# Performance work log

Measured on AMD Instinct MI355X. Metric: run time of the kernel, lower is better.

## Reference

```python
import jax, jax.numpy as jnp
import numpy as np

# dims (see shape_source): seq S = d_t+1 must equal d_k for the unary quantum loader
B, T, D_IN = 128, 127, 48
DK = 128
S = T + 1            # tokens incl. class token; S == DK
H, L = 8, 6
P = (S * S - S) // 2  # RBS angles per head (pyramid circuit over S wires)


def _pyramid_pairs(n):
    # deterministic pyramid ordering of n(n-1)/2 adjacent-pair Givens rotations
    a, b = [], []
    for k in range(n - 1):
        for i in range(k, -1, -1):
            a.append(i)
            b.append(i + 1)
    return np.asarray(a, np.int32), np.asarray(b, np.int32)


def _build_W(phi, pa, pb, n):
    # classical simulation of the RBS pyramid circuit restricted to the unary
    # subspace: product of Givens rotations -> orthogonal n x n matrix
    def step(W, inp):
        ia, ib, th = inp
        c, s = jnp.cos(th), jnp.sin(th)
        ra, rb = W[ia], W[ib]
        W = W.at[ia].set(c * ra - s * rb)
        W = W.at[ib].set(s * ra + c * rb)
        return W, None
    W0 = jnp.eye(n, dtype=phi.dtype)
    W, _ = jax.lax.scan(step, W0, (pa, pb, phi))
    return W


def _layer_norm(x, g, b, eps=1e-5):
    m = jnp.mean(x, axis=-1, keepdims=True)
    v = jnp.mean((x - m) ** 2, axis=-1, keepdims=True)
    return (x - m) * jax.lax.rsqrt(v + eps) * g + b


def setup_inputs() -> dict:
    key = jax.random.key(0)
    ks = jax.random.split(key, 8)
    f32 = jnp.float32
    return {
        "x": jax.random.normal(ks[0], (B, T, D_IN), f32),
        "embed_w": jax.random.normal(ks[1], (DK, D_IN), f32) / np.sqrt(D_IN),
        "embed_b": jnp.zeros((DK,), f32),
        "class_token": jax.random.normal(ks[2], (DK,), f32) / DK,
        "norm0_g": jnp.ones((DK,), f32),
        "norm0_b": jnp.zeros((DK,), f32),
        "Vw": jax.random.normal(ks[3], (L, H, DK, DK), f32) / np.sqrt(DK),
        "Vb": jnp.zeros((L, H, DK), f32),
        "ln_g": jnp.ones((L, H, DK), f32),
        "ln_b": jnp.zeros((L, H, DK), f32),
        "phi": jax.random.normal(ks[4], (L, H, P), f32) / np.sqrt(S),
        "merger_w": jax.random.normal(ks[5], (L, H), f32) / np.sqrt(H),
        "merger_b": jnp.zeros((L,), f32),
    }


def reference(x, embed_w, embed_b, class_token, norm0_g, norm0_b,
              Vw, Vb, ln_g, ln_b, phi, merger_w, merger_b):
    Bsz = x.shape[0]
    pa, pb = _pyramid_pairs(S)
    # orthogonal score matrices for every (layer, head)
    Ws = jax.vmap(lambda p: _build_W(p, pa, pb, S))(phi.reshape(L * H, P))
    Ws = Ws.reshape(L, H, S, S)

    # embed patches, prepend class token (pos_embedding add is a no-op in the
    # original source: bare `+self.pos_embedding` statement, so it is omitted)
    tok = jnp.einsum('btf,df->btd', x, embed_w) + embed_b
    h = jnp.concatenate([jnp.broadcast_to(class_token, (Bsz, 1, DK)), tok], axis=1)
    h = _layer_norm(h, norm0_g, norm0_b)

    scale = 1.0 / np.sqrt(DK)
    for l in range(L):
        nrm = jnp.sqrt(jnp.sum(h * h, axis=-1))      # input3: token norms [B,S]
        u = h / nrm[..., None]                        # unit tokens (convert_array)
        hh, nn, uu = h, nrm, u

        def head(W, vw, vb, g, be):
            V = jnp.einsum('bsd,ed->bse', hh, vw) + vb
            M = jnp.einsum('bsd,de,bte->bst', uu, W, uu)
            A = (M * M) * (nn[:, :, None] * nn[:, None, :])
            Pm = jax.nn.softmax(A * scale, axis=-1)
            return _layer_norm(jnp.einsum('bst,btd->bsd', Pm, V) + hh, g, be)

        hs = jax.vmap(head)(Ws[l], Vw[l], Vb[l], ln_g[l], ln_b[l])  # [H,B,S,D]
        h = jnp.einsum('hbsd,h->bsd', hs, merger_w[l]) + merger_b[l]
    return h[:, -1, :]
```

## Files before the change

kernel.cpp:

```cpp
#include <hip/hip_runtime.h>
#include <hip/hip_bf16.h>


typedef __bf16 bf16x8 __attribute__((ext_vector_type(8)));
typedef float  f32x4  __attribute__((ext_vector_type(4)));
typedef unsigned int u32;

__device__ __forceinline__ int sidx(int row, int col)
{
    return row * 128 + ((((col >> 3) ^ (row & 15)) << 3) | (col & 7));
}

__global__ void __launch_bounds__(256)
prep_kernel(const float* __restrict__ phi, float2* __restrict__ csn,
            const float* __restrict__ vw,  __bf16* __restrict__ cvwf)
{
    if (blockIdx.x < 3072) {
        const int mat = blockIdx.x >> 6;
        const int t   = ((blockIdx.x & 63) << 2) + (threadIdx.x >> 6);
        const int j   = threadIdx.x & 63;
        float th = 0.f;
        if (t < 253) {
            const int p = t & 1, i = 2 * j + p;
            const int lim = min(t, 252 - t);
            if (i <= lim) {
                const int k = (t + i) >> 1;
                th = phi[mat * 8128 + ((k * (k + 1)) >> 1) + (k - i)];
            }
        }
        float sn, cs;
        __sincosf(th, &sn, &cs);
        csn[(mat * 256 + t) * 64 + j] = make_float2(cs, sn);
    } else {
        const int f    = (blockIdx.x - 3072) * 256 + threadIdx.x;
        const int lane = f & 63;
        const int k0   = (f >> 6) & 3;
        const int t    = (f >> 8) & 7;
        const int lh   = f >> 11;
        const int row  = t * 16 + (lane & 15);
        const int col  = k0 * 32 + (lane >> 4) * 8;
        const float* src = vw + (lh * 128 + row) * 128 + col;
        __bf16* dst = cvwf + f * 8;
#pragma unroll
        for (int j = 0; j < 8; j++) dst[j] = (__bf16)src[j];
    }
}

__global__ void __launch_bounds__(64)
build_w_kernel(const float2* __restrict__ csn, __bf16* __restrict__ wtf)
{
    const int mat = blockIdx.x >> 5;
    const int grp = blockIdx.x & 31;
    const int c0  = grp * 4;
    const int lam = threadIdx.x;

    const float2* base = csn + (mat * 256) * 64 + lam;

    float vlo[4], vhi[4];
#pragma unroll
    for (int j = 0; j < 4; j++) {
        vlo[j] = (2 * lam     == c0 + j) ? 1.f : 0.f;
        vhi[j] = (2 * lam + 1 == c0 + j) ? 1.f : 0.f;
    }

    float2 buf[3][16];
#pragma unroll
    for (int k = 0; k < 16; k++) buf[0][k] = base[k * 64];
#pragma unroll
    for (int k = 0; k < 16; k++) buf[1][k] = base[(16 + k) * 64];

#pragma unroll
    for (int g = 0; g < 16; g++) {
        const int cb = g % 3;
        if (g < 14) {
            const int nb = (g + 2) % 3;
#pragma unroll
            for (int k = 0; k < 16; k++)
                buf[nb][k] = base[((g + 2) * 16 + k) * 64];
        }
#pragma unroll
        for (int p = 0; p < 8; p++) {
            {
                const float cs = buf[cb][2 * p].x, sn = buf[cb][2 * p].y;
#pragma unroll
                for (int j = 0; j < 4; j++) {
                    float lo = vlo[j], hi = vhi[j];
                    vlo[j] = cs * lo - sn * hi;
                    vhi[j] = sn * lo + cs * hi;
                }
            }
            {
                const float cs = buf[cb][2 * p + 1].x, sn = buf[cb][2 * p + 1].y;
#pragma unroll
                for (int j = 0; j < 4; j++) {
                    float y  = __shfl_down(vlo[j], 1);
                    float x  = vhi[j];
                    float xn = cs * x - sn * y;
                    float yn = sn * x + cs * y;
                    vhi[j] = xn;
                    float z = __shfl_up(yn, 1);
                    if (lam > 0) vlo[j] = z;
                }
            }
        }
    }

    u32* wtu = (u32*)wtf;
#pragma unroll
    for (int j = 0; j < 4; j++) {
        const int c = c0 + j;
        __bf16 va = (__bf16)vlo[j];
        __bf16 vb = (__bf16)vhi[j];
        u32 pk = (u32)__builtin_bit_cast(unsigned short, va)
               | ((u32)__builtin_bit_cast(unsigned short, vb) << 16);
        const int idx = (((c >> 4) * 4 + (lam >> 4)) * 64
                         + ((lam >> 2) & 3) * 16 + (c & 15)) * 4 + (lam & 3);
        wtu[mat * 8192 + idx] = pk;
    }
}

__global__ void __launch_bounds__(512)
embed_kernel(const float* __restrict__ x,  const float* __restrict__ ew,
             const float* __restrict__ eb, const float* __restrict__ ct,
             const float* __restrict__ g0, const float* __restrict__ b0,
             float* __restrict__ hf, __bf16* __restrict__ hb,
             float* __restrict__ invn)
{
    __shared__ float sx[4][48];
    __shared__ float sred[4][2];
    const int d  = threadIdx.x & 127, sq = threadIdx.x >> 7;
    const int wh = (threadIdx.x >> 6) & 1;
    const int b  = blockIdx.x & 127;
    const int s  = (blockIdx.x >> 7) * 4 + sq;

    if (s > 0 && d < 48) sx[sq][d] = x[(b * 127 + (s - 1)) * 48 + d];
    __syncthreads();

    float val;
    if (s == 0) {
        val = ct[d];
    } else {
        float aa = 0.f;
#pragma unroll
        for (int f = 0; f < 48; f++) aa = fmaf(sx[sq][f], ew[d * 48 + f], aa);
        val = aa + eb[d];
    }
    float v = val;
#pragma unroll
    for (int m = 32; m; m >>= 1) v += __shfl_xor(v, m);
    if ((threadIdx.x & 63) == 0) sred[sq][wh] = v;
    __syncthreads();
    float mean = (sred[sq][0] + sred[sq][1]) * (1.f / 128.f);
    float xc   = val - mean;
    __syncthreads();
    v = xc * xc;
#pragma unroll
    for (int m = 32; m; m >>= 1) v += __shfl_xor(v, m);
    if ((threadIdx.x & 63) == 0) sred[sq][wh] = v;
    __syncthreads();
    float var = (sred[sq][0] + sred[sq][1]) * (1.f / 128.f);
    float y   = xc * rsqrtf(var + 1e-5f) * g0[d] + b0[d];
    __syncthreads();
    v = y * y;
#pragma unroll
    for (int m = 32; m; m >>= 1) v += __shfl_xor(v, m);
    if ((threadIdx.x & 63) == 0) sred[sq][wh] = v;
    __syncthreads();
    float ss = sred[sq][0] + sred[sq][1];

    const int o = (b * 128 + s) * 128 + d;
    hf[o] = y;
    hb[o] = (__bf16)y;
    if (d == 0) invn[b * 128 + s] = rsqrtf(ss);
}

__global__ void __launch_bounds__(512, 4)
attn_kernel(int l,
            const float*  __restrict__ hf,  const __bf16* __restrict__ hb,
            const float*  __restrict__ invn, const __bf16* __restrict__ wtf,
            const __bf16* __restrict__ vwf, const float* __restrict__ vb,
            const float* __restrict__ lng,  const float* __restrict__ lnb,
            const float* __restrict__ mwp,  __bf16* __restrict__ hs)
{
    __shared__ __align__(16) __bf16 sH[128 * 128];
    __shared__ __align__(16) __bf16 sY[128 * 128];
    __shared__ float sInv[128];
    __shared__ float sVb[128];
    __shared__ float sLg[128];
    __shared__ float sLb[128];

    const int tid  = threadIdx.x;
    const int lane = tid & 63, w = tid >> 6;
    const int l15  = lane & 15, quad = lane >> 4;
    const int b    = blockIdx.x & 127;
    const int hh   = blockIdx.x >> 7;
    const int lh   = l * 8 + hh;

    const __bf16* hbp = hb + b * 16384;

#pragma unroll
    for (int c = 0; c < 4; c++) {
        int ch  = tid + c * 512;
        int row = ch >> 4, cc = ch & 15;
        bf16x8 hv = *(const bf16x8*)(hbp + ch * 8);
        *(bf16x8*)(&sH[sidx(row, cc * 8)]) = hv;
    }
    if (tid < 128) {
        sInv[tid] = invn[b * 128 + tid];
        sVb[tid]  = vb[lh * 128 + tid];
        sLg[tid]  = lng[lh * 128 + tid];
        sLb[tid]  = lnb[lh * 128 + tid];
    }
    __syncthreads();

    const int r0 = w * 16;
    const int kq = quad * 8;
    const int q4 = quad * 4;
    const f32x4 vzero = {0.f, 0.f, 0.f, 0.f};

    f32x4 acc[8];

    auto mmG = [&](const __bf16* gbase) {
#pragma unroll
        for (int t = 0; t < 8; t++) acc[t] = vzero;
        const __bf16* gp = gbase + lane * 8;
#pragma unroll
        for (int k0c = 0; k0c < 4; k0c++) {
            bf16x8 a0 = *(const bf16x8*)(&sH[sidx(r0 + l15, k0c * 32 + kq)]);
#pragma unroll
            for (int t = 0; t < 8; t++) {
                bf16x8 bb = *(const bf16x8*)(gp + (t * 4 + k0c) * 512);
                acc[t] = __builtin_amdgcn_mfma_f32_16x16x32_bf16(a0, bb, acc[t], 0, 0, 0);
            }
        }
    };
    auto mmL = [&]() {
#pragma unroll
        for (int t = 0; t < 8; t++) acc[t] = vzero;
#pragma unroll
        for (int k0 = 0; k0 < 128; k0 += 32) {
            const int kk = k0 + kq;
            bf16x8 a0 = *(const bf16x8*)(&sY[sidx(r0 + l15, kk)]);
#pragma unroll
            for (int t = 0; t < 8; t++) {
                bf16x8 bb = *(const bf16x8*)(&sH[sidx(t * 16 + l15, kk)]);
                acc[t] = __builtin_amdgcn_mfma_f32_16x16x32_bf16(a0, bb, acc[t], 0, 0, 0);
            }
        }
    };

    mmG(wtf + (size_t)lh * 16384);
#pragma unroll
    for (int t = 0; t < 8; t++)
#pragma unroll
        for (int r = 0; r < 4; r++)
            sY[sidx(r0 + q4 + r, t * 16 + l15)] = (__bf16)acc[t][r];

    mmL();

    {
        const float scale2 = 0.08838834764831843f * 1.4426950408889634f;
        float invt[8];
#pragma unroll
        for (int t = 0; t < 8; t++) invt[t] = sInv[t * 16 + l15];
        float invs[4];
#pragma unroll
        for (int r = 0; r < 4; r++) invs[r] = sInv[r0 + q4 + r];

        float mx[4] = {-3e38f, -3e38f, -3e38f, -3e38f};
#pragma unroll
        for (int t = 0; t < 8; t++)
#pragma unroll
            for (int r = 0; r < 4; r++) {
                float g = acc[t][r];
                float v = g * g * invs[r] * invt[t] * scale2;
                acc[t][r] = v;
                mx[r] = fmaxf(mx[r], v);
            }
#pragma unroll
        for (int m = 1; m < 16; m <<= 1)
#pragma unroll
            for (int r = 0; r < 4; r++) mx[r] = fmaxf(mx[r], __shfl_xor(mx[r], m));

        float sm[4] = {0.f, 0.f, 0.f, 0.f};
#pragma unroll
        for (int t = 0; t < 8; t++)
#pragma unroll
            for (int r = 0; r < 4; r++) {
                float e = exp2f(acc[t][r] - mx[r]);
                acc[t][r] = e;
                sm[r] += e;
            }
#pragma unroll
        for (int m = 1; m < 16; m <<= 1)
#pragma unroll
            for (int r = 0; r < 4; r++) sm[r] += __shfl_xor(sm[r], m);
#pragma unroll
        for (int r = 0; r < 4; r++) sm[r] = 1.0f / sm[r];
#pragma unroll
        for (int t = 0; t < 8; t++)
#pragma unroll
            for (int r = 0; r < 4; r++)
                sY[sidx(r0 + q4 + r, t * 16 + l15)] = (__bf16)(acc[t][r] * sm[r]);
    }

    float hres[8][4];
    {
        const float* hfp = hf + (b * 128 + r0 + q4) * 128;
#pragma unroll
        for (int t = 0; t < 8; t++)
#pragma unroll
            for (int r = 0; r < 4; r++)
                hres[t][r] = hfp[r * 128 + t * 16 + l15];
    }

    mmG(vwf + (size_t)lh * 16384);
    __syncthreads();

    {
        float vbv[8];
#pragma unroll
        for (int t = 0; t < 8; t++) vbv[t] = sVb[t * 16 + l15];
#pragma unroll
        for (int t = 0; t < 8; t++)
#pragma unroll
            for (int r = 0; r < 4; r++)
                sH[sidx(t * 16 + l15, r0 + q4 + r)] = (__bf16)(acc[t][r] + vbv[t]);
    }
    __syncthreads();

    mmL();

    {
        const float mw = mwp[lh];
        float lgv[8], lbv[8];
#pragma unroll
        for (int t = 0; t < 8; t++) {
            lgv[t] = sLg[t * 16 + l15];
            lbv[t] = sLb[t * 16 + l15];
        }
        float sum_[4] = {0.f, 0.f, 0.f, 0.f};
        float sq_[4]  = {0.f, 0.f, 0.f, 0.f};
#pragma unroll
        for (int t = 0; t < 8; t++)
#pragma unroll
            for (int r = 0; r < 4; r++) {
                float xx = acc[t][r] + hres[t][r];
                acc[t][r] = xx;
                sum_[r] += xx;
                sq_[r]  += xx * xx;
            }
#pragma unroll
        for (int m = 1; m < 16; m <<= 1)
#pragma unroll
            for (int r = 0; r < 4; r++) {
                sum_[r] += __shfl_xor(sum_[r], m);
                sq_[r]  += __shfl_xor(sq_[r], m);
            }
        float mean[4], rstd[4];
#pragma unroll
        for (int r = 0; r < 4; r++) {
            mean[r] = sum_[r] * (1.f / 128.f);
            float var = sq_[r] * (1.f / 128.f) - mean[r] * mean[r];
            rstd[r] = rsqrtf(fmaxf(var, 0.f) + 1e-5f);
        }
        __bf16* hsp = hs + ((hh * 128 + b) * 128 + r0 + q4) * 128;
#pragma unroll
        for (int t = 0; t < 8; t++)
#pragma unroll
            for (int r = 0; r < 4; r++) {
                float y = (acc[t][r] - mean[r]) * rstd[r] * lgv[t] + lbv[t];
                hsp[r * 128 + t * 16 + l15] = (__bf16)(y * mw);
            }
    }
}

static __device__ __forceinline__ float block_sum_128(float v, float* sred)
{
#pragma unroll
    for (int m = 32; m; m >>= 1) v += __shfl_xor(v, m);
    __syncthreads();
    if ((threadIdx.x & 63) == 0) sred[threadIdx.x >> 6] = v;
    __syncthreads();
    return sred[0] + sred[1];
}

__global__ void __launch_bounds__(128)
merge_kernel(const __bf16* __restrict__ hs, const float* __restrict__ mbp, int l,
             float* __restrict__ hf, __bf16* __restrict__ hb, float* __restrict__ invn,
             float* __restrict__ out, int last)
{
    __shared__ float sred[2];
    const int b = blockIdx.x & 127, s = blockIdx.x >> 7, d = threadIdx.x;

    float acc = mbp[l];
#pragma unroll
    for (int h = 0; h < 8; h++)
        acc += (float)hs[((h * 128 + b) * 128 + s) * 128 + d];

    float ss = block_sum_128(acc * acc, sred);

    const int o = (b * 128 + s) * 128 + d;
    hf[o] = acc;
    hb[o] = (__bf16)acc;
    if (d == 0) invn[b * 128 + s] = rsqrtf(ss);
    if (last && s == 127) out[b * 128 + d] = acc;
}

extern "C" void kernel_launch(void* const* d_in, const int* in_sizes, int n_in,
                              void* d_out, int out_size, void* d_ws, size_t ws_size,
                              hipStream_t stream)
{
    (void)in_sizes; (void)n_in; (void)out_size; (void)ws_size;

    const float* x   = (const float*)d_in[0];
    const float* ew  = (const float*)d_in[1];
    const float* eb  = (const float*)d_in[2];
    const float* ct  = (const float*)d_in[3];
    const float* g0  = (const float*)d_in[4];
    const float* b0  = (const float*)d_in[5];
    const float* vw  = (const float*)d_in[6];
    const float* vb  = (const float*)d_in[7];
    const float* lng = (const float*)d_in[8];
    const float* lnb = (const float*)d_in[9];
    const float* phi = (const float*)d_in[10];
    const float* mw  = (const float*)d_in[11];
    const float* mb  = (const float*)d_in[12];
    float* out = (float*)d_out;

    char* ws = (char*)d_ws;
    __bf16* wtf  = (__bf16*)(ws);
    float*  hf   = (float*)(ws + 1572864);
    __bf16* hb   = (__bf16*)(ws + 9961472);
    float*  invn = (float*)(ws + 14155776);
    __bf16* hs   = (__bf16*)(ws + 14221312);
    __bf16* cvwf = (__bf16*)(ws + 47775744);
    float2* csn  = (float2*)(ws + 49348608);

    prep_kernel<<<3456, 256, 0, stream>>>(phi, csn, vw, cvwf);
    build_w_kernel<<<1536, 64, 0, stream>>>(csn, wtf);
    embed_kernel<<<4096, 512, 0, stream>>>(x, ew, eb, ct, g0, b0, hf, hb, invn);
    for (int l = 0; l < 6; l++) {
        attn_kernel<<<1024, 512, 0, stream>>>(l, hf, hb, invn, wtf, cvwf, vb,
                                              lng, lnb, mw, hs);
        merge_kernel<<<16384, 128, 0, stream>>>(hs, mb, l, hf, hb, invn, out,
                                                (l == 5) ? 1 : 0);
    }
}
```

Measured before the change: 463.4 us.

## Stage rotation matrix in LDS for first GEMM and widen merge kernel work per block

The build kernel now writes W transposed in a plain row-major layout instead of MFMA fragment order. The attention kernel loads W into shared memory alongside H at kernel start and computes H·W from LDS rather than streaming fragments from global memory. This adds a barrier before overwriting sY. The merge kernel now handles four tokens per 256-thread block with two elements per thread, dropping the shared-memory block reduction in favour of a single wave shuffle and using vectorised stores.

```diff
diff --git a/kernel.cpp b/kernel.cpp
--- a/kernel.cpp
+++ b/kernel.cpp
@@ -42,12 +42,12 @@
         const float* src = vw + (lh * 128 + row) * 128 + col;
         __bf16* dst = cvwf + f * 8;
 #pragma unroll
-        for (int j = 0; j < 8; j++) dst[j] = (__bf16)src[j];
+        for (int j2 = 0; j2 < 8; j2++) dst[j2] = (__bf16)src[j2];
     }
 }
 
 __global__ void __launch_bounds__(64)
-build_w_kernel(const float2* __restrict__ csn, __bf16* __restrict__ wtf)
+build_w_kernel(const float2* __restrict__ csn, __bf16* __restrict__ wt)
 {
     const int mat = blockIdx.x >> 5;
     const int grp = blockIdx.x & 31;
@@ -105,17 +105,14 @@
         }
     }
 
-    u32* wtu = (u32*)wtf;
+    u32* wtu = (u32*)wt;
 #pragma unroll
     for (int j = 0; j < 4; j++) {
-        const int c = c0 + j;
         __bf16 va = (__bf16)vlo[j];
         __bf16 vb = (__bf16)vhi[j];
         u32 pk = (u32)__builtin_bit_cast(unsigned short, va)
                | ((u32)__builtin_bit_cast(unsigned short, vb) << 16);
-        const int idx = (((c >> 4) * 4 + (lam >> 4)) * 64
-                         + ((lam >> 2) & 3) * 16 + (c & 15)) * 4 + (lam & 3);
-        wtu[mat * 8192 + idx] = pk;
+        wtu[mat * 8192 + (c0 + j) * 64 + lam] = pk;
     }
 }
 
@@ -177,7 +174,7 @@
 __global__ void __launch_bounds__(512, 4)
 attn_kernel(int l,
             const float*  __restrict__ hf,  const __bf16* __restrict__ hb,
-            const float*  __restrict__ invn, const __bf16* __restrict__ wtf,
+            const float*  __restrict__ invn, const __bf16* __restrict__ wt,
             const __bf16* __restrict__ vwf, const float* __restrict__ vb,
             const float* __restrict__ lng,  const float* __restrict__ lnb,
             const float* __restrict__ mwp,  __bf16* __restrict__ hs)
@@ -197,13 +194,16 @@
     const int lh   = l * 8 + hh;
 
     const __bf16* hbp = hb + b * 16384;
+    const __bf16* wtp = wt + lh * 16384;
 
 #pragma unroll
     for (int c = 0; c < 4; c++) {
         int ch  = tid + c * 512;
         int row = ch >> 4, cc = ch & 15;
         bf16x8 hv = *(const bf16x8*)(hbp + ch * 8);
+        bf16x8 wv = *(const bf16x8*)(wtp + ch * 8);
         *(bf16x8*)(&sH[sidx(row, cc * 8)]) = hv;
+        *(bf16x8*)(&sY[sidx(row, cc * 8)]) = wv;
     }
     if (tid < 128) {
         sInv[tid] = invn[b * 128 + tid];
@@ -220,43 +220,30 @@
 
     f32x4 acc[8];
 
-    auto mmG = [&](const __bf16* gbase) {
-#pragma unroll
-        for (int t = 0; t < 8; t++) acc[t] = vzero;
-        const __bf16* gp = gbase + lane * 8;
-#pragma unroll
-        for (int k0c = 0; k0c < 4; k0c++) {
-            bf16x8 a0 = *(const bf16x8*)(&sH[sidx(r0 + l15, k0c * 32 + kq)]);
-#pragma unroll
-            for (int t = 0; t < 8; t++) {
-                bf16x8 bb = *(const bf16x8*)(gp + (t * 4 + k0c) * 512);
-                acc[t] = __builtin_amdgcn_mfma_f32_16x16x32_bf16(a0, bb, acc[t], 0, 0, 0);
-            }
-        }
-    };
-    auto mmL = [&]() {
+    auto mmL = [&](const __bf16* Ab, const __bf16* Bb) {
 #pragma unroll
         for (int t = 0; t < 8; t++) acc[t] = vzero;
 #pragma unroll
         for (int k0 = 0; k0 < 128; k0 += 32) {
             const int kk = k0 + kq;
-            bf16x8 a0 = *(const bf16x8*)(&sY[sidx(r0 + l15, kk)]);
+            bf16x8 a0 = *(const bf16x8*)(&Ab[sidx(r0 + l15, kk)]);
 #pragma unroll
             for (int t = 0; t < 8; t++) {
-                bf16x8 bb = *(const bf16x8*)(&sH[sidx(t * 16 + l15, kk)]);
+                bf16x8 bb = *(const bf16x8*)(&Bb[sidx(t * 16 + l15, kk)]);
                 acc[t] = __builtin_amdgcn_mfma_f32_16x16x32_bf16(a0, bb, acc[t], 0, 0, 0);
             }
         }
     };
 
-    mmG(wtf + (size_t)lh * 16384);
+    mmL(sH, sY);
+    __syncthreads();
 #pragma unroll
     for (int t = 0; t < 8; t++)
 #pragma unroll
         for (int r = 0; r < 4; r++)
             sY[sidx(r0 + q4 + r, t * 16 + l15)] = (__bf16)acc[t][r];
 
-    mmL();
+    mmL(sY, sH);
 
     {
         const float scale2 = 0.08838834764831843f * 1.4426950408889634f;
@@ -314,7 +301,21 @@
                 hres[t][r] = hfp[r * 128 + t * 16 + l15];
     }
 
-    mmG(vwf + (size_t)lh * 16384);
+    {
+        const __bf16* vbase = vwf + (size_t)lh * 16384;
+#pragma unroll
+        for (int t = 0; t < 8; t++) acc[t] = vzero;
+#pragma unroll
+        for (int k0c = 0; k0c < 4; k0c++) {
+            const int kk = k0c * 32 + kq;
+            bf16x8 a0 = *(const bf16x8*)(&sH[sidx(r0 + l15, kk)]);
+#pragma unroll
+            for (int t = 0; t < 8; t++) {
+                bf16x8 bb = *(const bf16x8*)(vbase + ((t * 4 + k0c) * 64 + lane) * 8);
+                acc[t] = __builtin_amdgcn_mfma_f32_16x16x32_bf16(a0, bb, acc[t], 0, 0, 0);
+            }
+        }
+    }
     __syncthreads();
 
     {
@@ -329,7 +330,7 @@
     }
     __syncthreads();
 
-    mmL();
+    mmL(sY, sH);
 
     {
         const float mw = mwp[lh];
@@ -375,36 +376,35 @@
     }
 }
 
-static __device__ __forceinline__ float block_sum_128(float v, float* sred)
-{
-#pragma unroll
-    for (int m = 32; m; m >>= 1) v += __shfl_xor(v, m);
-    __syncthreads();
-    if ((threadIdx.x & 63) == 0) sred[threadIdx.x >> 6] = v;
-    __syncthreads();
-    return sred[0] + sred[1];
-}
-
-__global__ void __launch_bounds__(128)
+__global__ void __launch_bounds__(256)
 merge_kernel(const __bf16* __restrict__ hs, const float* __restrict__ mbp, int l,
              float* __restrict__ hf, __bf16* __restrict__ hb, float* __restrict__ invn,
              float* __restrict__ out, int last)
 {
-    __shared__ float sred[2];
-    const int b = blockIdx.x & 127, s = blockIdx.x >> 7, d = threadIdx.x;
-
-    float acc = mbp[l];
-#pragma unroll
-    for (int h = 0; h < 8; h++)
-        acc += (float)hs[((h * 128 + b) * 128 + s) * 128 + d];
-
-    float ss = block_sum_128(acc * acc, sred);
-
-    const int o = (b * 128 + s) * 128 + d;
-    hf[o] = acc;
-    hb[o] = (__bf16)acc;
-    if (d == 0) invn[b * 128 + s] = rsqrtf(ss);
-    if (last && s == 127) out[b * 128 + d] = acc;
+    const int b  = blockIdx.x & 127;
+    const int s  = (blockIdx.x >> 7) * 4 + (threadIdx.x >> 6);
+    const int ln = threadIdx.x & 63;
+    const int d2 = ln * 2;
+
+    const float mbv = mbp[l];
+    float a0 = mbv, a1 = mbv;
+#pragma unroll
+    for (int h8 = 0; h8 < 8; h8++) {
+        const __bf16* p = hs + (((size_t)h8 * 128 + b) * 128 + s) * 128 + d2;
+        a0 += (float)p[0];
+        a1 += (float)p[1];
+    }
+    float v = a0 * a0 + a1 * a1;
+#pragma unroll
+    for (int m = 32; m; m >>= 1) v += __shfl_xor(v, m);
+
+    const size_t o = ((size_t)b * 128 + s) * 128 + d2;
+    *(float2*)(hf + o) = make_float2(a0, a1);
+    __bf16 p0 = (__bf16)a0, p1 = (__bf16)a1;
+    ((u32*)hb)[o >> 1] = (u32)__builtin_bit_cast(unsigned short, p0)
+                       | ((u32)__builtin_bit_cast(unsigned short, p1) << 16);
+    if (ln == 0) invn[b * 128 + s] = rsqrtf(v);
+    if (last && s == 127) *(float2*)(out + b * 128 + d2) = make_float2(a0, a1);
 }
 
 extern "C" void kernel_launch(void* const* d_in, const int* in_sizes, int n_in,
@@ -429,7 +429,7 @@
     float* out = (float*)d_out;
 
     char* ws = (char*)d_ws;
-    __bf16* wtf  = (__bf16*)(ws);
+    __bf16* wt   = (__bf16*)(ws);
     float*  hf   = (float*)(ws + 1572864);
     __bf16* hb   = (__bf16*)(ws + 9961472);
     float*  invn = (float*)(ws + 14155776);
@@ -438,12 +438,12 @@
     float2* csn  = (float2*)(ws + 49348608);
 
     prep_kernel<<<3456, 256, 0, stream>>>(phi, csn, vw, cvwf);
-    build_w_kernel<<<1536, 64, 0, stream>>>(csn, wtf);
+    build_w_kernel<<<1536, 64, 0, stream>>>(csn, wt);
     embed_kernel<<<4096, 512, 0, stream>>>(x, ew, eb, ct, g0, b0, hf, hb, invn);
     for (int l = 0; l < 6; l++) {
-        attn_kernel<<<1024, 512, 0, stream>>>(l, hf, hb, invn, wtf, cvwf, vb,
+        attn_kernel<<<1024, 512, 0, stream>>>(l, hf, hb, invn, wt, cvwf, vb,
                                               lng, lnb, mw, hs);
-        merge_kernel<<<16384, 128, 0, stream>>>(hs, mb, l, hf, hb, invn, out,
-                                                (l == 5) ? 1 : 0);
-    }
-}
+        merge_kernel<<<4096, 256, 0, stream>>>(hs, mb, l, hf, hb, invn, out,
+                                               (l == 5) ? 1 : 0);
+    }
+}
```

After: 422.1 us (median of 2 runs). 8.9% less time.
